# Optimization experiments

Hardware: AMD Instinct MI355X
Metric: run time of the kernel (lower is better)

The kernel has to match this reference:

```python
import jax, jax.numpy as jnp
import numpy as np

B, L, D, H = 4, 2048, 2048, 16
HEAD_DIM = D // H
EPS = 1e-5


def rmsnorm(x, w):
    # fp32 RMSNorm as in the torch module
    xf = x.astype(jnp.float32)
    rms = jnp.sqrt(jnp.mean(xf * xf, axis=-1, keepdims=True) + EPS)
    return xf / rms * w


def apply_rope(x, freqs):
    # x: (..., D) with interleaved even/odd pairs; freqs: (2, L, D/2) = (sin, cos)
    sin, cos = freqs[0], freqs[1]
    xr = x.reshape(*x.shape[:-1], D // 2, 2)
    x_even, x_odd = xr[..., 0], xr[..., 1]
    e = x_even * cos - x_odd * sin
    o = x_odd * cos + x_even * sin
    return jnp.stack([e, o], axis=-1).reshape(x.shape)


def setup_inputs() -> dict:
    key = jax.random.key(0)
    k0, k1, k2 = jax.random.split(key, 3)
    x_BLD = jax.random.normal(k0, (B, L, D), dtype=jnp.float32)
    # realistic RoPE angle table over the full dim (matches module usage)
    t = jnp.arange(L, dtype=jnp.float32)[:, None]
    inv_freq = 1.0 / (10000.0 ** (jnp.arange(D // 2, dtype=jnp.float32) / (D // 2)))
    ang = t * inv_freq[None, :]                      # (L, D/2)
    freqs = jnp.stack([jnp.sin(ang), jnp.cos(ang)])  # (2, L, D/2)
    wqkv = jax.random.normal(k1, (3 * D, D), dtype=jnp.float32) * 0.02
    wo = jax.random.normal(k2, (D, D), dtype=jnp.float32) * 0.02
    q_norm_w = jnp.ones((D,), dtype=jnp.float32)
    k_norm_w = jnp.ones((D,), dtype=jnp.float32)
    return {"x_BLD": x_BLD, "freqs": freqs, "wqkv": wqkv, "wo": wo,
            "q_norm_w": q_norm_w, "k_norm_w": k_norm_w}


def reference(x_BLD, freqs, wqkv, wo, q_norm_w, k_norm_w):
    dtype = x_BLD.dtype
    qkv = x_BLD @ wqkv.T                             # (B, L, 3D)
    q, k, v = jnp.split(qkv, 3, axis=-1)
    q = apply_rope(rmsnorm(q, q_norm_w), freqs).astype(dtype)
    k = apply_rope(rmsnorm(k, k_norm_w), freqs).astype(dtype)
    # (B, L, D) -> (B, H, L, hd)
    q = q.reshape(B, L, H, HEAD_DIM).transpose(0, 2, 1, 3)
    k = k.reshape(B, L, H, HEAD_DIM).transpose(0, 2, 1, 3)
    v = v.reshape(B, L, H, HEAD_DIM).transpose(0, 2, 1, 3)
    scale = HEAD_DIM ** -0.5
    scores = jnp.einsum('bhqd,bhkd->bhqk', q, k) * scale
    attn = jax.nn.softmax(scores, axis=-1)
    out = jnp.einsum('bhqk,bhkd->bhqd', attn, v)
    out = out.transpose(0, 2, 1, 3).reshape(B, L, D)
    return out @ wo.T
```

## Files before the change

### kernel.cpp

```cpp
#include <hip/hip_runtime.h>
#include <stdint.h>
#include <stddef.h>

typedef unsigned short u16;
typedef __bf16 bf16x8 __attribute__((ext_vector_type(8)));
typedef __bf16 bf16x2 __attribute__((ext_vector_type(2)));
typedef float  f32x4  __attribute__((ext_vector_type(4)));
typedef float  f32x16 __attribute__((ext_vector_type(16)));

__device__ __forceinline__ float bf2f(u16 u){ return __uint_as_float(((unsigned)u)<<16); }
__device__ __forceinline__ u16 f2bf(float f){
  unsigned u = __float_as_uint(f);
  return (u16)((u + 0x7fffu + ((u>>16)&1u)) >> 16);
}
__device__ __forceinline__ void gl_lds16(const void* g, void* s){
  __builtin_amdgcn_global_load_lds(
      (__attribute__((address_space(1))) void*)(void*)g,
      (__attribute__((address_space(3))) void*)s, 16, 0, 0);
}

__global__ void k_f2bf(const float* __restrict__ in, u16* __restrict__ out, int n4){
  int i = blockIdx.x*256 + threadIdx.x;
  if (i < n4){
    float4 v = ((const float4*)in)[i];
    ((ushort4*)out)[i] = make_ushort4(f2bf(v.x), f2bf(v.y), f2bf(v.z), f2bf(v.w));
  }
}

#define BAR()  do{ __asm__ __volatile__("" ::: "memory"); \
                   __builtin_amdgcn_s_barrier(); \
                   __asm__ __volatile__("" ::: "memory"); }while(0)
#define VMC6()  __asm__ __volatile__("s_waitcnt vmcnt(6)" ::: "memory")
#define VMC0()  __asm__ __volatile__("s_waitcnt vmcnt(0)" ::: "memory")

#define STAGE_A(B_,H_,T_) do{ \
  const u16* _s = A + (size_t)(m0 + (H_)*128 + w16 + sr)*K + (T_)*64 + sc; \
  gl_lds16(_s,               &As[B_][H_][w16*64]); \
  gl_lds16(_s + (size_t)8*K, &As[B_][H_][(w16+8)*64]); }while(0)
#define STAGE_B(B_,H_,T_) do{ \
  const u16* _s = Bm + (size_t)(n0 + (H_)*128 + w16 + sr)*K + (T_)*64 + sc; \
  gl_lds16(_s,               &Bs[B_][H_][w16*64]); \
  gl_lds16(_s + (size_t)8*K, &Bs[B_][H_][(w16+8)*64]); }while(0)

#define RD_A2(P_,B_) do{ \
  _Pragma("unroll") for (int i_=0; i_<2; ++i_){ \
    int r_ = wm*64 + (2*((P_)&1)+i_)*16 + l16; \
    const u16* p_ = &As[B_][(P_)>>1][r_*64]; \
    af[i_][0] = *(const bf16x8*)&p_[(( quad    ^ (r_&7))<<3)]; \
    af[i_][1] = *(const bf16x8*)&p_[(((quad+4) ^ (r_&7))<<3)]; } }while(0)
#define RD_B8(B_) do{ \
  _Pragma("unroll") for (int j_=0; j_<4; ++j_){ \
    int r_ = wn*32 + (j_&1)*16 + l16; \
    const u16* p_ = &Bs[B_][j_>>1][r_*64]; \
    bfr[j_][0] = *(const bf16x8*)&p_[(( quad    ^ (r_&7))<<3)]; \
    bfr[j_][1] = *(const bf16x8*)&p_[(((quad+4) ^ (r_&7))<<3)]; } }while(0)

#define MM_P(P_) do{ \
  __builtin_amdgcn_sched_barrier(0); \
  __builtin_amdgcn_s_setprio(1); \
  _Pragma("unroll") for (int k_=0;k_<2;++k_) \
    _Pragma("unroll") for (int i_=0;i_<2;++i_) \
      _Pragma("unroll") for (int j_=0;j_<4;++j_) \
        acc[P_][i_][j_] = __builtin_amdgcn_mfma_f32_16x16x32_bf16( \
            af[i_][k_], bfr[j_][k_], acc[P_][i_][j_], 0,0,0); \
  __builtin_amdgcn_s_setprio(0); \
  __builtin_amdgcn_sched_barrier(0); }while(0)

#define TILE(B_,X_,T_,S1_,S2_,S3_,VM_) do{ \
  RD_A2(0,B_); RD_B8(B_);                                        BAR(); MM_P(0); \
  RD_A2(1,B_); if(S1_){STAGE_A(X_,1,(T_)+1);}                    BAR(); MM_P(1); \
  RD_A2(2,B_); if(S2_){STAGE_B(B_,0,(T_)+2);STAGE_B(B_,1,(T_)+2);} BAR(); MM_P(2); \
  RD_A2(3,B_); if(S3_){STAGE_A(B_,0,(T_)+2);} VM_;               BAR(); MM_P(3); \
}while(0)

template<int BF16OUT>
__global__ __launch_bounds__(512,2) void k_gemm256(const u16* __restrict__ A,
                                                   const u16* __restrict__ Bm,
                                                   void* __restrict__ Cout,
                                                   int M, int N, int K){
  __shared__ __align__(16) u16 As[2][2][128*64];
  __shared__ __align__(16) u16 Bs[2][2][128*64];
  const int tid = threadIdx.x, w = tid>>6, ln = tid&63;
  const int l16 = ln&15, quad = ln>>4;
  const int wm = w&1, wn = w>>1;
  const int w16 = w*16, sr = ln>>3;
  const int sc = ((ln&7) ^ sr) << 3;
  const int nbx = N>>8;
  const int nwg = nbx*(M>>8);
  const int lid = blockIdx.y*nbx + blockIdx.x;
  const int swz = (lid&7)*(nwg>>3) + (lid>>3);
  const int m0 = (swz/nbx)<<8, n0 = (swz%nbx)<<8;

  f32x4 acc[4][2][4];
  #pragma unroll
  for (int a=0;a<4;++a)
    #pragma unroll
    for (int b=0;b<2;++b)
      #pragma unroll
      for (int c=0;c<4;++c){ acc[a][b][c][0]=0.f; acc[a][b][c][1]=0.f;
                             acc[a][b][c][2]=0.f; acc[a][b][c][3]=0.f; }
  bf16x8 af[2][2], bfr[4][2];

  STAGE_B(0,0,0); STAGE_B(0,1,0); STAGE_A(0,0,0); STAGE_A(0,1,0);
  STAGE_B(1,0,1); STAGE_B(1,1,1); STAGE_A(1,0,1);
  VMC6(); BAR();

  const int niter = (K>>7) - 1;
  for (int j=0; j<niter; ++j){
    const int t0 = 2*j;
    TILE(0,1,t0,   1,1,1, VMC6());
    TILE(1,0,t0+1, 1,1,1, VMC6());
  }
  {
    const int t0 = K>>6;
    TILE(0,1,t0-2, 1,0,0, VMC0());
    TILE(1,0,t0-1, 0,0,0, );
  }
  #pragma unroll
  for (int p=0;p<4;++p)
    #pragma unroll
    for (int i=0;i<2;++i)
      #pragma unroll
      for (int jj=0;jj<4;++jj)
        #pragma unroll
        for (int r=0;r<4;++r){
          int row = m0 + (p>>1)*128 + wm*64 + (2*(p&1)+i)*16 + quad*4 + r;
          int col = n0 + (jj>>1)*128 + wn*32 + (jj&1)*16 + l16;
          if (BF16OUT) ((u16*)Cout)[(size_t)row*N + col] = f2bf(acc[p][i][jj][r]);
          else         ((float*)Cout)[(size_t)row*N + col] = acc[p][i][jj][r];
        }
}

__global__ void k_prep_qk(const u16* __restrict__ qkv, const float* __restrict__ freqs,
                          const float* __restrict__ qw, const float* __restrict__ kw,
                          u16* __restrict__ Qo, u16* __restrict__ Ko){
  const int row = blockIdx.x;
  const int b = row >> 11, l = row & 2047;
  const int tid = threadIdx.x;
  const u16* qr = qkv + (size_t)row*6144;
  float qe[4], qo[4], ke[4], ko_[4];
  float sq = 0.f, sk = 0.f;
  #pragma unroll
  for (int it=0; it<4; ++it){
    int p = tid + it*256;
    ushort2 q2 = ((const ushort2*)qr)[p];
    ushort2 k2 = ((const ushort2*)(qr+2048))[p];
    qe[it]=bf2f(q2.x); qo[it]=bf2f(q2.y);
    ke[it]=bf2f(k2.x); ko_[it]=bf2f(k2.y);
    sq += qe[it]*qe[it] + qo[it]*qo[it];
    sk += ke[it]*ke[it] + ko_[it]*ko_[it];
  }
  #pragma unroll
  for (int off=32; off; off>>=1){ sq += __shfl_xor(sq, off); sk += __shfl_xor(sk, off); }
  __shared__ float red[8];
  if ((tid&63)==0){ red[tid>>6]=sq; red[4+(tid>>6)]=sk; }
  __syncthreads();
  sq = red[0]+red[1]+red[2]+red[3];
  sk = red[4]+red[5]+red[6]+red[7];
  const float rq = rsqrtf(sq*(1.f/2048.f) + 1e-5f);
  const float rk = rsqrtf(sk*(1.f/2048.f) + 1e-5f);
  const float QS = 0.08838834764831845f * 1.4426950408889634f;
  #pragma unroll
  for (int it=0; it<4; ++it){
    int p = tid + it*256;
    float sn = freqs[(size_t)l*1024 + p];
    float cs = freqs[2097152 + (size_t)l*1024 + p];
    float2 w2q = ((const float2*)qw)[p];
    float2 w2k = ((const float2*)kw)[p];
    int h = p>>6, dd2 = p&63;
    size_t o = ((size_t)(b*16+h)*2048 + l)*64 + dd2;
    float a = qe[it]*rq*w2q.x, c = qo[it]*rq*w2q.y;
    ((ushort2*)Qo)[o] = make_ushort2(f2bf((a*cs - c*sn)*QS), f2bf((c*cs + a*sn)*QS));
    a = ke[it]*rk*w2k.x; c = ko_[it]*rk*w2k.y;
    ((ushort2*)Ko)[o] = make_ushort2(f2bf(a*cs - c*sn), f2bf(c*cs + a*sn));
  }
}

__global__ void k_prep_v(const u16* __restrict__ qkv, u16* __restrict__ Vt){
  const int lt = blockIdx.x, bh = blockIdx.y;
  const int b = bh>>4, h = bh&15;
  __shared__ u16 tile[64][136];
  const int tid = threadIdx.x;
  #pragma unroll
  for (int it=0; it<32; ++it){
    int idx = it*256 + tid;
    int lo = idx >> 7, dd = idx & 127;
    tile[lo][dd] = qkv[(size_t)(b*2048 + lt*64 + lo)*6144 + 4096 + h*128 + dd];
  }
  __syncthreads();
  #pragma unroll
  for (int it=0; it<32; ++it){
    int idx = it*256 + tid;
    int dd = idx >> 6, lo = idx & 63;
    Vt[((size_t)bh*128 + dd)*2048 + lt*64 + lo] = tile[lo][dd];
  }
}

__global__ __launch_bounds__(256,2) void k_flash(const u16* __restrict__ Q,
                                                 const u16* __restrict__ Kg,
                                                 const u16* __restrict__ Vt,
                                                 u16* __restrict__ O){
  __shared__ __align__(16) u16 Kt[128*136];
  __shared__ __align__(16) u16 Vs[128*136];
  const int qt = blockIdx.x, bh = blockIdx.y;
  const int tid = threadIdx.x, w = tid>>6, ln = tid&63;
  const int l31 = ln&31, hi = ln>>5;
  const int b = bh>>4, h = bh&15;
  const size_t qkbase = (size_t)bh*(2048*128);

  const int srow = tid>>4, scol = tid&15;
  const u16* kgp = Kg + qkbase + (size_t)srow*128 + scol*8;
  const u16* vgp = Vt + (size_t)bh*(128*2048) + (size_t)srow*2048 + scol*8;
  u16* kld = &Kt[srow*136 + scol*8];
  u16* vld = &Vs[srow*136 + scol*8];

  bf16x8 qf[8];
  {
    const u16* qp = Q + qkbase + (size_t)(qt*128 + w*32 + l31)*128 + hi*8;
    #pragma unroll
    for (int kk=0; kk<8; ++kk) qf[kk] = *(const bf16x8*)(qp + kk*16);
  }

  union U4 { unsigned u[4]; bf16x8 v; };
  U4 uones; uones.u[0]=0x3F803F80u; uones.u[1]=0x3F803F80u;
  uones.u[2]=0x3F803F80u; uones.u[3]=0x3F803F80u;
  const bf16x8 ones = uones.v;

  f32x16 o[4], o4;
  #pragma unroll
  for (int dt=0; dt<4; ++dt)
    #pragma unroll
    for (int r=0; r<16; ++r) o[dt][r] = 0.f;
  #pragma unroll
  for (int r=0; r<16; ++r) o4[r] = 0.f;

  bf16x8 kreg[8], vreg[8];
  #pragma unroll
  for (int it=0; it<8; ++it) kreg[it] = *(const bf16x8*)(kgp + (size_t)it*16*128);
  #pragma unroll
  for (int it=0; it<8; ++it) vreg[it] = *(const bf16x8*)(vgp + (size_t)it*16*2048);

  for (int kt=0; kt<16; ++kt){
    __syncthreads();
    #pragma unroll
    for (int it=0; it<8; ++it) *(bf16x8*)(kld + it*16*136) = kreg[it];
    #pragma unroll
    for (int it=0; it<8; ++it) *(bf16x8*)(vld + it*16*136) = vreg[it];
    __syncthreads();
    if (kt < 15){
      #pragma unroll
      for (int it=0; it<8; ++it)
        kreg[it] = *(const bf16x8*)(kgp + (size_t)(kt+1)*128*128 + (size_t)it*16*128);
      #pragma unroll
      for (int it=0; it<8; ++it)
        vreg[it] = *(const bf16x8*)(vgp + (kt+1)*128 + (size_t)it*16*2048);
    }
    f32x16 s[4];
    #pragma unroll
    for (int t=0;t<4;++t)
      #pragma unroll
      for (int r=0;r<16;++r) s[t][r] = 0.f;
    #pragma unroll
    for (int kk=0; kk<8; ++kk){
      #pragma unroll
      for (int t=0; t<4; ++t){
        bf16x8 a = *(const bf16x8*)&Kt[(t*32 + l31)*136 + kk*16 + hi*8];
        s[t] = __builtin_amdgcn_mfma_f32_32x32x16_bf16(a, qf[kk], s[t], 0,0,0);
      }
    }
    bf16x8 bfrag[8];
    #pragma unroll
    for (int t=0;t<4;++t){
      unsigned pk[4][2];
      #pragma unroll
      for (int g=0;g<4;++g){
        float p0 = exp2f(s[t][g*4+0]);
        float p1 = exp2f(s[t][g*4+1]);
        float p2 = exp2f(s[t][g*4+2]);
        float p3 = exp2f(s[t][g*4+3]);
        bf16x2 c01, c23;
        c01[0] = (__bf16)p0; c01[1] = (__bf16)p1;
        c23[0] = (__bf16)p2; c23[1] = (__bf16)p3;
        pk[g][0] = __builtin_bit_cast(unsigned, c01);
        pk[g][1] = __builtin_bit_cast(unsigned, c23);
      }
      auto r0 = __builtin_amdgcn_permlane32_swap((int)pk[0][0], (int)pk[1][0], false, false);
      auto r1 = __builtin_amdgcn_permlane32_swap((int)pk[0][1], (int)pk[1][1], false, false);
      auto r2 = __builtin_amdgcn_permlane32_swap((int)pk[2][0], (int)pk[3][0], false, false);
      auto r3 = __builtin_amdgcn_permlane32_swap((int)pk[2][1], (int)pk[3][1], false, false);
      U4 u0, u1;
      u0.u[0] = (unsigned)r0[0]; u0.u[1] = (unsigned)r1[0];
      u0.u[2] = (unsigned)r0[1]; u0.u[3] = (unsigned)r1[1];
      u1.u[0] = (unsigned)r2[0]; u1.u[1] = (unsigned)r3[0];
      u1.u[2] = (unsigned)r2[1]; u1.u[3] = (unsigned)r3[1];
      bfrag[t*2+0] = u0.v;
      bfrag[t*2+1] = u1.v;
    }
    #pragma unroll
    for (int kk=0; kk<8; ++kk){
      #pragma unroll
      for (int dt=0; dt<4; ++dt){
        bf16x8 a = *(const bf16x8*)&Vs[(dt*32 + l31)*136 + kk*16 + hi*8];
        o[dt] = __builtin_amdgcn_mfma_f32_32x32x16_bf16(a, bfrag[kk], o[dt], 0,0,0);
      }
      o4 = __builtin_amdgcn_mfma_f32_32x32x16_bf16(ones, bfrag[kk], o4, 0,0,0);
    }
  }
  const float inv = 1.f/o4[0];
  __syncthreads();
  #pragma unroll
  for (int dt=0;dt<4;++dt)
    #pragma unroll
    for (int g=0;g<4;++g)
      *(ushort4*)&Kt[(w*32+l31)*136 + dt*32 + g*8 + hi*4] =
        make_ushort4(f2bf(o[dt][g*4+0]*inv), f2bf(o[dt][g*4+1]*inv),
                     f2bf(o[dt][g*4+2]*inv), f2bf(o[dt][g*4+3]*inv));
  __syncthreads();
  #pragma unroll
  for (int it=0; it<8; ++it){
    int q = it*16 + srow;
    bf16x8 vv = *(const bf16x8*)&Kt[q*136 + scol*8];
    *(bf16x8*)&O[(size_t)(b*2048 + qt*128 + q)*2048 + h*128 + scol*8] = vv;
  }
}

extern "C" void kernel_launch(void* const* d_in, const int* in_sizes, int n_in,
                              void* d_out, int out_size, void* d_ws, size_t ws_size,
                              hipStream_t stream){
  const float* x     = (const float*)d_in[0];
  const float* freqs = (const float*)d_in[1];
  const float* wqkv  = (const float*)d_in[2];
  const float* wo    = (const float*)d_in[3];
  const float* qw    = (const float*)d_in[4];
  const float* kw    = (const float*)d_in[5];
  char* ws = (char*)d_ws;
  u16* xbf    = (u16*)(ws);
  u16* wqkvbf = (u16*)(ws + 33554432);
  u16* wobf   = (u16*)(ws + 58720256);
  u16* qkvbf  = (u16*)(ws + 67108864);
  u16* Qbf    = (u16*)(ws + 167772160);
  u16* Kbf    = (u16*)(ws + 201326592);
  u16* Vtbf   = (u16*)(ws + 234881024);
  u16* Abf    = qkvbf;
  float* out  = (float*)d_out;

  k_f2bf<<<16384,256,0,stream>>>(x,    xbf,    4194304);
  k_f2bf<<<12288,256,0,stream>>>(wqkv, wqkvbf, 3145728);
  k_f2bf<<< 4096,256,0,stream>>>(wo,   wobf,   1048576);
  k_gemm256<1><<<dim3(24,32),512,0,stream>>>(xbf, wqkvbf, qkvbf, 8192, 6144, 2048);
  k_prep_qk<<<8192,256,0,stream>>>(qkvbf, freqs, qw, kw, Qbf, Kbf);
  k_prep_v<<<dim3(32,64),256,0,stream>>>(qkvbf, Vtbf);
  k_flash<<<dim3(16,64),256,0,stream>>>(Qbf, Kbf, Vtbf, Abf);
  k_gemm256<0><<<dim3(8,32),512,0,stream>>>(Abf, wobf, out, 8192, 2048, 2048);
}
```

Measured before the change: 643.8 us.

## Pre-swizzle V into MFMA fragment layout and load V fragments directly from global

k_prep_v now writes V in a per-128-key-tile layout that matches the MFMA A-operand fragment order, using 16-byte vector loads and stores. The flash kernel reads V fragments straight from global (L2) into registers, with no LDS staging. This removes the Vs shared buffer and its stores, halving LDS use. The row sum is now accumulated with scalar adds plus a cross-half shuffle instead of an extra MFMA against a ones vector. In exchange, global traffic per block rises and latency is less hidden, since the V loads are issued within the same iteration instead of prefetched a tile ahead.

```diff
diff --git a/kernel.cpp b/kernel.cpp
--- a/kernel.cpp
+++ b/kernel.cpp
@@ -177,22 +177,28 @@
 }
 
 __global__ void k_prep_v(const u16* __restrict__ qkv, u16* __restrict__ Vt){
-  const int lt = blockIdx.x, bh = blockIdx.y;
+  const int kt = blockIdx.x, bh = blockIdx.y;
   const int b = bh>>4, h = bh&15;
-  __shared__ u16 tile[64][136];
+  __shared__ __align__(16) u16 tile[128][136];
   const int tid = threadIdx.x;
   #pragma unroll
-  for (int it=0; it<32; ++it){
-    int idx = it*256 + tid;
-    int lo = idx >> 7, dd = idx & 127;
-    tile[lo][dd] = qkv[(size_t)(b*2048 + lt*64 + lo)*6144 + 4096 + h*128 + dd];
+  for (int it=0; it<8; ++it){
+    int c  = it*256 + tid;
+    int lo = c >> 4, c8 = (c & 15) << 3;
+    *(bf16x8*)&tile[lo][c8] =
+      *(const bf16x8*)&qkv[(size_t)(b*2048 + kt*128 + lo)*6144 + 4096 + h*128 + c8];
   }
   __syncthreads();
-  #pragma unroll
-  for (int it=0; it<32; ++it){
-    int idx = it*256 + tid;
-    int dd = idx >> 6, lo = idx & 63;
-    Vt[((size_t)bh*128 + dd)*2048 + lt*64 + lo] = tile[lo][dd];
+  union V8 { u16 s[8]; bf16x8 v; };
+  u16* vo = Vt + (size_t)(bh*16 + kt)*16384;
+  #pragma unroll
+  for (int it=0; it<8; ++it){
+    int c  = it*256 + tid;
+    int d  = c & 127, hb = c >> 7;
+    V8 u;
+    #pragma unroll
+    for (int j=0;j<8;++j) u.s[j] = tile[hb*8 + j][d];
+    *(bf16x8*)&vo[(size_t)hb*1024 + d*8] = u.v;
   }
 }
 
@@ -201,7 +207,6 @@
                                                  const u16* __restrict__ Vt,
                                                  u16* __restrict__ O){
   __shared__ __align__(16) u16 Kt[128*136];
-  __shared__ __align__(16) u16 Vs[128*136];
   const int qt = blockIdx.x, bh = blockIdx.y;
   const int tid = threadIdx.x, w = tid>>6, ln = tid&63;
   const int l31 = ln&31, hi = ln>>5;
@@ -210,9 +215,8 @@
 
   const int srow = tid>>4, scol = tid&15;
   const u16* kgp = Kg + qkbase + (size_t)srow*128 + scol*8;
-  const u16* vgp = Vt + (size_t)bh*(128*2048) + (size_t)srow*2048 + scol*8;
   u16* kld = &Kt[srow*136 + scol*8];
-  u16* vld = &Vs[srow*136 + scol*8];
+  const u16* vb = Vt + (size_t)bh*16*16384 + hi*1024 + l31*8;
 
   bf16x8 qf[8];
   {
@@ -222,39 +226,34 @@
   }
 
   union U4 { unsigned u[4]; bf16x8 v; };
-  U4 uones; uones.u[0]=0x3F803F80u; uones.u[1]=0x3F803F80u;
-  uones.u[2]=0x3F803F80u; uones.u[3]=0x3F803F80u;
-  const bf16x8 ones = uones.v;
-
-  f32x16 o[4], o4;
+
+  f32x16 o[4];
   #pragma unroll
   for (int dt=0; dt<4; ++dt)
     #pragma unroll
     for (int r=0; r<16; ++r) o[dt][r] = 0.f;
-  #pragma unroll
-  for (int r=0; r<16; ++r) o4[r] = 0.f;
-
-  bf16x8 kreg[8], vreg[8];
+  float l_ = 0.f;
+
+  bf16x8 kreg[8];
   #pragma unroll
   for (int it=0; it<8; ++it) kreg[it] = *(const bf16x8*)(kgp + (size_t)it*16*128);
-  #pragma unroll
-  for (int it=0; it<8; ++it) vreg[it] = *(const bf16x8*)(vgp + (size_t)it*16*2048);
 
   for (int kt=0; kt<16; ++kt){
     __syncthreads();
     #pragma unroll
     for (int it=0; it<8; ++it) *(bf16x8*)(kld + it*16*136) = kreg[it];
-    #pragma unroll
-    for (int it=0; it<8; ++it) *(bf16x8*)(vld + it*16*136) = vreg[it];
     __syncthreads();
     if (kt < 15){
       #pragma unroll
       for (int it=0; it<8; ++it)
         kreg[it] = *(const bf16x8*)(kgp + (size_t)(kt+1)*128*128 + (size_t)it*16*128);
-      #pragma unroll
-      for (int it=0; it<8; ++it)
-        vreg[it] = *(const bf16x8*)(vgp + (kt+1)*128 + (size_t)it*16*2048);
     }
+    const u16* vt_k = vb + (size_t)kt*16384;
+    bf16x8 vf0[8], vf1[8];
+    #pragma unroll
+    for (int kk=0; kk<8; ++kk) vf0[kk] = *(const bf16x8*)(vt_k + kk*2048);
+    #pragma unroll
+    for (int kk=0; kk<8; ++kk) vf1[kk] = *(const bf16x8*)(vt_k + kk*2048 + 256);
     f32x16 s[4];
     #pragma unroll
     for (int t=0;t<4;++t)
@@ -268,6 +267,7 @@
         s[t] = __builtin_amdgcn_mfma_f32_32x32x16_bf16(a, qf[kk], s[t], 0,0,0);
       }
     }
+    float rs = 0.f;
     bf16x8 bfrag[8];
     #pragma unroll
     for (int t=0;t<4;++t){
@@ -278,6 +278,7 @@
         float p1 = exp2f(s[t][g*4+1]);
         float p2 = exp2f(s[t][g*4+2]);
         float p3 = exp2f(s[t][g*4+3]);
+        rs += (p0+p1)+(p2+p3);
         bf16x2 c01, c23;
         c01[0] = (__bf16)p0; c01[1] = (__bf16)p1;
         c23[0] = (__bf16)p2; c23[1] = (__bf16)p3;
@@ -296,17 +297,22 @@
       bfrag[t*2+0] = u0.v;
       bfrag[t*2+1] = u1.v;
     }
+    rs += __shfl_xor(rs, 32);
+    l_ += rs;
+    bf16x8 vf2[8], vf3[8];
+    #pragma unroll
+    for (int kk=0; kk<8; ++kk) vf2[kk] = *(const bf16x8*)(vt_k + kk*2048 + 512);
+    #pragma unroll
+    for (int kk=0; kk<8; ++kk) vf3[kk] = *(const bf16x8*)(vt_k + kk*2048 + 768);
     #pragma unroll
     for (int kk=0; kk<8; ++kk){
-      #pragma unroll
-      for (int dt=0; dt<4; ++dt){
-        bf16x8 a = *(const bf16x8*)&Vs[(dt*32 + l31)*136 + kk*16 + hi*8];
-        o[dt] = __builtin_amdgcn_mfma_f32_32x32x16_bf16(a, bfrag[kk], o[dt], 0,0,0);
-      }
-      o4 = __builtin_amdgcn_mfma_f32_32x32x16_bf16(ones, bfrag[kk], o4, 0,0,0);
+      o[0] = __builtin_amdgcn_mfma_f32_32x32x16_bf16(vf0[kk], bfrag[kk], o[0], 0,0,0);
+      o[1] = __builtin_amdgcn_mfma_f32_32x32x16_bf16(vf1[kk], bfrag[kk], o[1], 0,0,0);
+      o[2] = __builtin_amdgcn_mfma_f32_32x32x16_bf16(vf2[kk], bfrag[kk], o[2], 0,0,0);
+      o[3] = __builtin_amdgcn_mfma_f32_32x32x16_bf16(vf3[kk], bfrag[kk], o[3], 0,0,0);
     }
   }
-  const float inv = 1.f/o4[0];
+  const float inv = 1.f/l_;
   __syncthreads();
   #pragma unroll
   for (int dt=0;dt<4;++dt)
@@ -349,7 +355,7 @@
   k_f2bf<<< 4096,256,0,stream>>>(wo,   wobf,   1048576);
   k_gemm256<1><<<dim3(24,32),512,0,stream>>>(xbf, wqkvbf, qkvbf, 8192, 6144, 2048);
   k_prep_qk<<<8192,256,0,stream>>>(qkvbf, freqs, qw, kw, Qbf, Kbf);
-  k_prep_v<<<dim3(32,64),256,0,stream>>>(qkvbf, Vtbf);
+  k_prep_v<<<dim3(16,64),256,0,stream>>>(qkvbf, Vtbf);
   k_flash<<<dim3(16,64),256,0,stream>>>(Qbf, Kbf, Vtbf, Abf);
   k_gemm256<0><<<dim3(8,32),512,0,stream>>>(Abf, wobf, out, 8192, 2048, 2048);
 }
```

Result: faster. 610.7 us (-5.1%).
